# Performance work log

Measured on AMD Instinct MI355X. Metric: run time of the kernel, lower is better.

The kernel has to match this reference:

```python
import jax, jax.numpy as jnp
import numpy as np

N = 50000
E = 800000
IN_CH = 128
OUT_CH = 128
HEADS = 4
HEAD_DIM = OUT_CH // HEADS  # 32
NEG_SLOPE = 0.2
BN_EPS = 1e-5


def setup_inputs() -> dict:
    key = jax.random.key(0)
    ks = jax.random.split(key, 12)
    s = 1.0 / np.sqrt(IN_CH)
    x = jax.random.normal(ks[0], (N, IN_CH), dtype=jnp.float32)
    edge_index = jax.random.randint(ks[1], (2, E), 0, N, dtype=jnp.int64)
    # GATv2 lin_l (source) and lin_r (target) weights + biases
    W_l = jax.random.uniform(ks[2], (IN_CH, HEADS * HEAD_DIM), jnp.float32, -s, s)
    b_l = jax.random.uniform(ks[3], (HEADS * HEAD_DIM,), jnp.float32, -s, s)
    W_r = jax.random.uniform(ks[4], (IN_CH, HEADS * HEAD_DIM), jnp.float32, -s, s)
    b_r = jax.random.uniform(ks[5], (HEADS * HEAD_DIM,), jnp.float32, -s, s)
    att = jax.random.uniform(ks[6], (HEADS, HEAD_DIM), jnp.float32, -s, s)
    bias = jnp.zeros((HEADS * HEAD_DIM,), jnp.float32)
    gamma = jnp.ones((OUT_CH,), jnp.float32)
    beta = jnp.zeros((OUT_CH,), jnp.float32)
    return {"x": x, "edge_index": edge_index, "W_l": W_l, "b_l": b_l,
            "W_r": W_r, "b_r": b_r, "att": att, "bias": bias,
            "gamma": gamma, "beta": beta}


def gatv2_layer(x, edge_index, W_l, b_l, W_r, b_r, att, bias, gamma, beta):
    # transformed source/target features: [N, H, C]
    x_l = (x @ W_l + b_l).reshape(N, HEADS, HEAD_DIM)
    x_r = (x @ W_r + b_r).reshape(N, HEADS, HEAD_DIM)
    # add self loops
    loop = jnp.arange(N, dtype=edge_index.dtype)
    src = jnp.concatenate([edge_index[0], loop])
    dst = jnp.concatenate([edge_index[1], loop])
    # GATv2 attention scores per edge: a^T LeakyReLU(x_j + x_i)  -> [Etot, H]
    e = jax.nn.leaky_relu(x_l[src] + x_r[dst], NEG_SLOPE)
    score = jnp.einsum('ehc,hc->eh', e, att)
    # segment softmax over incoming edges of each destination node
    m = jax.ops.segment_max(score, dst, num_segments=N)
    ex = jnp.exp(score - m[dst])
    denom = jax.ops.segment_sum(ex, dst, num_segments=N)
    alpha = ex / denom[dst]
    # scatter-add aggregation of alpha * x_l[src]
    out = jax.ops.segment_sum(alpha[:, :, None] * x_l[src], dst, num_segments=N)
    out = out.reshape(N, OUT_CH) + bias
    # BatchNorm over nodes (training-mode batch statistics)
    mu = jnp.mean(out, axis=0)
    var = jnp.var(out, axis=0)
    out = (out - mu) / jnp.sqrt(var + BN_EPS) * gamma + beta
    # residual (in_channels == out_channels -> identity path) + ELU
    out = jax.nn.elu(out + x)
    return out


def reference(x, edge_index, W_l, b_l, W_r, b_r, att, bias, gamma, beta):
    return gatv2_layer(x, edge_index, W_l, b_l, W_r, b_r, att, bias, gamma, beta)
```

## Files before the change

kernel.cpp:

```cpp
#include <hip/hip_runtime.h>

#define NN 50000
#define EE 800000
#define ETOT (EE + NN)
#define GEMM_GRID 512
#define MTILES 782
#define COUNT_BLOCKS 3125
#define AGG_BLOCKS 1563
#define SCAN_BLOCKS 196

typedef __attribute__((ext_vector_type(8))) short bhalf8;
typedef __attribute__((ext_vector_type(4))) float fx4;

__device__ __forceinline__ unsigned bf16r(float f) {
  unsigned u = __float_as_uint(f);
  return (u + 0x7FFFu + ((u >> 16) & 1u)) >> 16;
}

__device__ __forceinline__ float4 unpack_bf16x4(unsigned a, unsigned b) {
  float4 f;
  f.x = __uint_as_float(a << 16);
  f.y = __uint_as_float(a & 0xFFFF0000u);
  f.z = __uint_as_float(b << 16);
  f.w = __uint_as_float(b & 0xFFFF0000u);
  return f;
}

__global__ __launch_bounds__(256) void gemm_count(
    const float* __restrict__ x,
    const float* __restrict__ Wl, const float* __restrict__ bl,
    const float* __restrict__ Wr, const float* __restrict__ br,
    unsigned short* __restrict__ xlh, float* __restrict__ xr,
    const int* __restrict__ ei, int* __restrict__ deg) {
  if (blockIdx.x >= GEMM_GRID) {
    int e = (blockIdx.x - GEMM_GRID) * 256 + threadIdx.x;
    if (e < EE) atomicAdd(&deg[ei[EE + e]], 1);
    return;
  }
  const int t = threadIdx.x;
  const int w = t >> 6;
  const int l = t & 63;
  const int cl = l & 15;
  const int kb = (l >> 4) * 8;
  const int rsub = (l >> 4) * 4;

  bhalf8 bfr[4][4];
  float biasv[4];
#pragma unroll
  for (int nt = 0; nt < 4; ++nt) {
    int col = w * 64 + nt * 16 + cl;
    const float* Wsrc;
    if (col < 128) { Wsrc = Wl + col; biasv[nt] = bl[col]; }
    else           { Wsrc = Wr + (col - 128); biasv[nt] = br[col - 128]; }
#pragma unroll
    for (int ch = 0; ch < 4; ++ch) {
      int k0 = ch * 32 + kb;
      bhalf8 f;
#pragma unroll
      for (int j = 0; j < 8; ++j)
        f[j] = (short)bf16r(Wsrc[(size_t)(k0 + j) * 128]);
      bfr[nt][ch] = f;
    }
  }

  for (int mt = blockIdx.x; mt < MTILES; mt += GEMM_GRID) {
    const int m0 = mt * 64;
#pragma unroll
    for (int rt = 0; rt < 4; ++rt) {
      int row = m0 + rt * 16 + cl;
      int rowc = row < NN ? row : NN - 1;
      const float* xp = x + (size_t)rowc * 128 + kb;
      bhalf8 afr[4];
#pragma unroll
      for (int ch = 0; ch < 4; ++ch) {
        float4 q0 = *(const float4*)(xp + ch * 32);
        float4 q1 = *(const float4*)(xp + ch * 32 + 4);
        bhalf8 f;
        f[0] = (short)bf16r(q0.x); f[1] = (short)bf16r(q0.y);
        f[2] = (short)bf16r(q0.z); f[3] = (short)bf16r(q0.w);
        f[4] = (short)bf16r(q1.x); f[5] = (short)bf16r(q1.y);
        f[6] = (short)bf16r(q1.z); f[7] = (short)bf16r(q1.w);
        afr[ch] = f;
      }
#pragma unroll
      for (int nt = 0; nt < 4; ++nt) {
        fx4 acc = {biasv[nt], biasv[nt], biasv[nt], biasv[nt]};
#pragma unroll
        for (int ch = 0; ch < 4; ++ch)
          acc = __builtin_amdgcn_mfma_f32_16x16x32_bf16(afr[ch], bfr[nt][ch],
                                                        acc, 0, 0, 0);
        int col = w * 64 + nt * 16 + cl;
        int rbase = m0 + rt * 16 + rsub;
        if (col < 128) {
#pragma unroll
          for (int r = 0; r < 4; ++r) {
            int rr = rbase + r;
            if (rr < NN) xlh[(size_t)rr * 128 + col] = (unsigned short)bf16r(acc[r]);
          }
        } else {
          int c2 = col - 128;
#pragma unroll
          for (int r = 0; r < 4; ++r) {
            int rr = rbase + r;
            if (rr < NN) xr[(size_t)rr * 128 + c2] = acc[r];
          }
        }
      }
    }
  }
}

__global__ __launch_bounds__(256) void scanA(const int* __restrict__ deg,
                                             int* __restrict__ bsum,
                                             float* __restrict__ bn) {
  __shared__ int s[256];
  int t = threadIdx.x;
  if (blockIdx.x == 0) bn[t] = 0.f;
  int i = blockIdx.x * 256 + t;
  s[t] = (i < NN) ? deg[i] : 0;
  __syncthreads();
#pragma unroll
  for (int off = 128; off > 0; off >>= 1) {
    if (t < off) s[t] += s[t + off];
    __syncthreads();
  }
  if (t == 0) bsum[blockIdx.x] = s[0];
}

__global__ __launch_bounds__(256) void scanB(const int* __restrict__ deg,
                                             const int* __restrict__ bsum,
                                             int* __restrict__ offs,
                                             int* __restrict__ cursor) {
  __shared__ int s[256];
  __shared__ int bpref;
  int t = threadIdx.x;
  int bid = blockIdx.x;
  int i = bid * 256 + t;
  int v = (i < NN) ? deg[i] : 0;
  s[t] = v;
  if (t == 0) {
    int r = 0;
    for (int k = 0; k < bid; ++k) r += bsum[k];
    bpref = r;
  }
  __syncthreads();
  for (int off = 1; off < 256; off <<= 1) {
    int u = (t >= off) ? s[t - off] : 0;
    __syncthreads();
    s[t] += u;
    __syncthreads();
  }
  int excl = s[t] - v + bpref;
  if (i <= NN) {
    offs[i] = excl;
    if (i < NN) cursor[i] = excl;
  }
}

__global__ void fill_csr(const int* __restrict__ ei, int* __restrict__ cursor,
                         int* __restrict__ csr) {
  int e = blockIdx.x * 256 + threadIdx.x;
  if (e >= ETOT) return;
  int s, d;
  if (e < EE) { s = ei[e]; d = ei[EE + e]; }
  else { s = e - EE; d = s; }
  int pos = atomicAdd(&cursor[d], 1);
  csr[pos] = s;
}

__global__ __launch_bounds__(256) void aggregate(
    const unsigned short* __restrict__ xlh, const float* __restrict__ xr,
    const int* __restrict__ offs, const int* __restrict__ csr,
    const float* __restrict__ att,
    float* __restrict__ out, float* __restrict__ bn) {
  __shared__ float sbn[256];
  int t = threadIdx.x;
  sbn[t] = 0.f;
  __syncthreads();
  const int lane = t & 63;
  const int gl = lane & 15;
  const int gb = lane & 48;
  const int c8 = gl * 8;
  const int gid = (blockIdx.x * 256 + t) >> 4;
  const int gstride = gridDim.x * 16;
  const float4 at0 = *(const float4*)&att[c8];
  const float4 at1 = *(const float4*)&att[c8 + 4];
  float4 bs0 = make_float4(0, 0, 0, 0), bs1 = make_float4(0, 0, 0, 0);
  float4 bq0 = make_float4(0, 0, 0, 0), bq1 = make_float4(0, 0, 0, 0);

  for (int node = gid; node < NN; node += gstride) {
    const float4 xr0 = *(const float4*)&xr[(size_t)node * 128 + c8];
    const float4 xr1 = *(const float4*)&xr[(size_t)node * 128 + c8 + 4];
    const int beg = offs[node];
    const int deg = offs[node + 1] - beg;
    float den = 0.f;
    float4 a0 = make_float4(0, 0, 0, 0), a1 = make_float4(0, 0, 0, 0);

    for (int base = 0; base < deg; base += 16) {
      int cnt = deg - base; if (cnt > 16) cnt = 16;
      int msrc = (gl < cnt) ? csr[beg + base + gl] : 0;
      for (int eb = 0; eb < cnt; eb += 8) {
        uint4 u[8];
#pragma unroll
        for (int j = 0; j < 8; ++j) {
          int s = __shfl(msrc, gb + eb + j, 64);
          u[j] = *(const uint4*)(xlh + (size_t)s * 128 + c8);
        }
#pragma unroll
        for (int j = 0; j < 8; ++j) {
          float4 v0 = unpack_bf16x4(u[j].x, u[j].y);
          float4 v1 = unpack_bf16x4(u[j].z, u[j].w);
          float e, p;
          e = v0.x + xr0.x; e = e > 0.f ? e : 0.2f * e; p = e * at0.x;
          e = v0.y + xr0.y; e = e > 0.f ? e : 0.2f * e; p = fmaf(e, at0.y, p);
          e = v0.z + xr0.z; e = e > 0.f ? e : 0.2f * e; p = fmaf(e, at0.z, p);
          e = v0.w + xr0.w; e = e > 0.f ? e : 0.2f * e; p = fmaf(e, at0.w, p);
          e = v1.x + xr1.x; e = e > 0.f ? e : 0.2f * e; p = fmaf(e, at1.x, p);
          e = v1.y + xr1.y; e = e > 0.f ? e : 0.2f * e; p = fmaf(e, at1.y, p);
          e = v1.z + xr1.z; e = e > 0.f ? e : 0.2f * e; p = fmaf(e, at1.z, p);
          e = v1.w + xr1.w; e = e > 0.f ? e : 0.2f * e; p = fmaf(e, at1.w, p);
          p += __shfl_xor(p, 1);
          p += __shfl_xor(p, 2);
          float pe = (eb + j < cnt) ? __expf(p) : 0.f;
          den += pe;
          a0.x = fmaf(pe, v0.x, a0.x);
          a0.y = fmaf(pe, v0.y, a0.y);
          a0.z = fmaf(pe, v0.z, a0.z);
          a0.w = fmaf(pe, v0.w, a0.w);
          a1.x = fmaf(pe, v1.x, a1.x);
          a1.y = fmaf(pe, v1.y, a1.y);
          a1.z = fmaf(pe, v1.z, a1.z);
          a1.w = fmaf(pe, v1.w, a1.w);
        }
      }
    }

    float inv = 1.0f / den;
    float4 r0, r1;
    r0.x = a0.x * inv; r0.y = a0.y * inv; r0.z = a0.z * inv; r0.w = a0.w * inv;
    r1.x = a1.x * inv; r1.y = a1.y * inv; r1.z = a1.z * inv; r1.w = a1.w * inv;
    *(float4*)&out[(size_t)node * 128 + c8] = r0;
    *(float4*)&out[(size_t)node * 128 + c8 + 4] = r1;
    bs0.x += r0.x; bs0.y += r0.y; bs0.z += r0.z; bs0.w += r0.w;
    bs1.x += r1.x; bs1.y += r1.y; bs1.z += r1.z; bs1.w += r1.w;
    bq0.x += r0.x * r0.x; bq0.y += r0.y * r0.y; bq0.z += r0.z * r0.z; bq0.w += r0.w * r0.w;
    bq1.x += r1.x * r1.x; bq1.y += r1.y * r1.y; bq1.z += r1.z * r1.z; bq1.w += r1.w * r1.w;
  }

#define RED(F) F = F + __shfl_xor(F, 16); F = F + __shfl_xor(F, 32);
  RED(bs0.x) RED(bs0.y) RED(bs0.z) RED(bs0.w)
  RED(bs1.x) RED(bs1.y) RED(bs1.z) RED(bs1.w)
  RED(bq0.x) RED(bq0.y) RED(bq0.z) RED(bq0.w)
  RED(bq1.x) RED(bq1.y) RED(bq1.z) RED(bq1.w)
#undef RED
  if (lane < 16) {
    atomicAdd(&sbn[c8 + 0], bs0.x);
    atomicAdd(&sbn[c8 + 1], bs0.y);
    atomicAdd(&sbn[c8 + 2], bs0.z);
    atomicAdd(&sbn[c8 + 3], bs0.w);
    atomicAdd(&sbn[c8 + 4], bs1.x);
    atomicAdd(&sbn[c8 + 5], bs1.y);
    atomicAdd(&sbn[c8 + 6], bs1.z);
    atomicAdd(&sbn[c8 + 7], bs1.w);
    atomicAdd(&sbn[128 + c8 + 0], bq0.x);
    atomicAdd(&sbn[128 + c8 + 1], bq0.y);
    atomicAdd(&sbn[128 + c8 + 2], bq0.z);
    atomicAdd(&sbn[128 + c8 + 3], bq0.w);
    atomicAdd(&sbn[128 + c8 + 4], bq1.x);
    atomicAdd(&sbn[128 + c8 + 5], bq1.y);
    atomicAdd(&sbn[128 + c8 + 6], bq1.z);
    atomicAdd(&sbn[128 + c8 + 7], bq1.w);
  }
  __syncthreads();
  atomicAdd(&bn[t], sbn[t]);
}

__global__ __launch_bounds__(256) void finalize(
    float* __restrict__ out, const float* __restrict__ x,
    const float* __restrict__ bn, const float* __restrict__ gamma,
    const float* __restrict__ beta) {
  __shared__ float smu[128], sgi[128];
  int t = threadIdx.x;
  if (t < 128) {
    float mu = bn[t] * (1.0f / NN);
    float var = bn[128 + t] * (1.0f / NN) - mu * mu;
    smu[t] = mu;
    sgi[t] = rsqrtf(var + 1e-5f) * gamma[t];
  }
  __syncthreads();
  const int total4 = NN * 32;
  for (int i = blockIdx.x * blockDim.x + threadIdx.x; i < total4;
       i += gridDim.x * blockDim.x) {
    int c4 = (i & 31) * 4;
    float4 o = ((const float4*)out)[i];
    float4 xv = ((const float4*)x)[i];
    float4 mu = *(const float4*)&smu[c4];
    float4 gi = *(const float4*)&sgi[c4];
    float4 b4 = *(const float4*)&beta[c4];
    float v;
    v = (o.x - mu.x) * gi.x + b4.x + xv.x; o.x = v > 0.f ? v : expm1f(v);
    v = (o.y - mu.y) * gi.y + b4.y + xv.y; o.y = v > 0.f ? v : expm1f(v);
    v = (o.z - mu.z) * gi.z + b4.z + xv.z; o.z = v > 0.f ? v : expm1f(v);
    v = (o.w - mu.w) * gi.w + b4.w + xv.w; o.w = v > 0.f ? v : expm1f(v);
    ((float4*)out)[i] = o;
  }
}

extern "C" void kernel_launch(void* const* d_in, const int* in_sizes, int n_in,
                              void* d_out, int out_size, void* d_ws, size_t ws_size,
                              hipStream_t stream) {
  const float* x    = (const float*)d_in[0];
  const int*   ei   = (const int*)d_in[1];
  const float* Wl   = (const float*)d_in[2];
  const float* bl   = (const float*)d_in[3];
  const float* Wr   = (const float*)d_in[4];
  const float* br   = (const float*)d_in[5];
  const float* att  = (const float*)d_in[6];
  const float* gam  = (const float*)d_in[8];
  const float* bet  = (const float*)d_in[9];
  float* out = (float*)d_out;

  unsigned short* xlh = (unsigned short*)d_ws;
  float* xr   = (float*)(xlh + (size_t)NN * 128);
  int* offs   = (int*)(xr + (size_t)NN * 128);
  int* cursor = offs + (NN + 4);
  int* deg    = cursor + NN;
  int* csr    = deg + NN;
  float* bn   = (float*)(csr + ETOT);
  int* bsum   = (int*)(bn + 256);

  hipMemsetD32Async((hipDeviceptr_t)deg, 1, NN, stream);

  hipLaunchKernelGGL(gemm_count, dim3(GEMM_GRID + COUNT_BLOCKS), dim3(256), 0,
                     stream, x, Wl, bl, Wr, br, xlh, xr, ei, deg);
  hipLaunchKernelGGL(scanA, dim3(SCAN_BLOCKS), dim3(256), 0, stream, deg, bsum, bn);
  hipLaunchKernelGGL(scanB, dim3(SCAN_BLOCKS), dim3(256), 0, stream,
                     deg, bsum, offs, cursor);
  hipLaunchKernelGGL(fill_csr, dim3((ETOT + 255) / 256), dim3(256), 0, stream,
                     ei, cursor, csr);
  hipLaunchKernelGGL(aggregate, dim3(AGG_BLOCKS), dim3(256), 0, stream,
                     xlh, xr, offs, csr, att, out, bn);
  hipLaunchKernelGGL(finalize, dim3(2048), dim3(256), 0, stream, out, x, bn, gam, bet);
}
```

Measured before the change: 298.8 us.

## Double-buffer edge gathers in aggregation and stage GEMM weights through LDS

The aggregation loop now processes up to 32 edges per chunk and double-buffers the bf16 source-feature gathers, issuing the next batch of 8 loads before consuming the current one. This hides gather latency behind the score and accumulate math. The GEMM block now loads W_l/W_r coalesced into a transposed bf16 LDS tile instead of doing strided scalar global reads per lane. Grid sizes for the GEMM and aggregation kernels are also retuned. The changes add register pressure from two 8-entry uint4 buffers and about 68KB of LDS per GEMM block, which may lower occupancy.

```diff
diff --git a/kernel.cpp b/kernel.cpp
--- a/kernel.cpp
+++ b/kernel.cpp
@@ -3,10 +3,10 @@
 #define NN 50000
 #define EE 800000
 #define ETOT (EE + NN)
-#define GEMM_GRID 512
+#define GEMM_GRID 391
 #define MTILES 782
 #define COUNT_BLOCKS 3125
-#define AGG_BLOCKS 1563
+#define AGG_BLOCKS 1024
 #define SCAN_BLOCKS 196
 
 typedef __attribute__((ext_vector_type(8))) short bhalf8;
@@ -37,6 +37,7 @@
     if (e < EE) atomicAdd(&deg[ei[EE + e]], 1);
     return;
   }
+  __shared__ unsigned short sW[256 * 136];
   const int t = threadIdx.x;
   const int w = t >> 6;
   const int l = t & 63;
@@ -44,23 +45,33 @@
   const int kb = (l >> 4) * 8;
   const int rsub = (l >> 4) * 4;
 
+#pragma unroll
+  for (int it = 0; it < 16; ++it) {
+    int f4 = t + it * 256;
+    int k = f4 >> 5;
+    int c4 = (f4 & 31) * 4;
+    float4 v = *(const float4*)&Wl[(size_t)k * 128 + c4];
+    sW[(c4 + 0) * 136 + k] = (unsigned short)bf16r(v.x);
+    sW[(c4 + 1) * 136 + k] = (unsigned short)bf16r(v.y);
+    sW[(c4 + 2) * 136 + k] = (unsigned short)bf16r(v.z);
+    sW[(c4 + 3) * 136 + k] = (unsigned short)bf16r(v.w);
+    float4 u = *(const float4*)&Wr[(size_t)k * 128 + c4];
+    sW[(128 + c4 + 0) * 136 + k] = (unsigned short)bf16r(u.x);
+    sW[(128 + c4 + 1) * 136 + k] = (unsigned short)bf16r(u.y);
+    sW[(128 + c4 + 2) * 136 + k] = (unsigned short)bf16r(u.z);
+    sW[(128 + c4 + 3) * 136 + k] = (unsigned short)bf16r(u.w);
+  }
+  __syncthreads();
+
   bhalf8 bfr[4][4];
   float biasv[4];
 #pragma unroll
   for (int nt = 0; nt < 4; ++nt) {
     int col = w * 64 + nt * 16 + cl;
-    const float* Wsrc;
-    if (col < 128) { Wsrc = Wl + col; biasv[nt] = bl[col]; }
-    else           { Wsrc = Wr + (col - 128); biasv[nt] = br[col - 128]; }
-#pragma unroll
-    for (int ch = 0; ch < 4; ++ch) {
-      int k0 = ch * 32 + kb;
-      bhalf8 f;
-#pragma unroll
-      for (int j = 0; j < 8; ++j)
-        f[j] = (short)bf16r(Wsrc[(size_t)(k0 + j) * 128]);
-      bfr[nt][ch] = f;
-    }
+    biasv[nt] = (col < 128) ? bl[col] : br[col - 128];
+#pragma unroll
+    for (int ch = 0; ch < 4; ++ch)
+      bfr[nt][ch] = *(const bhalf8*)&sW[col * 136 + ch * 32 + kb];
   }
 
   for (int mt = blockIdx.x; mt < MTILES; mt += GEMM_GRID) {
@@ -188,6 +199,45 @@
   float4 bs0 = make_float4(0, 0, 0, 0), bs1 = make_float4(0, 0, 0, 0);
   float4 bq0 = make_float4(0, 0, 0, 0), bq1 = make_float4(0, 0, 0, 0);
 
+#define LOADB(buf, bb) do {                                                   \
+    int mm = ((bb) >= 2) ? m1 : m0;                                           \
+    int ebase = gb + (((bb) & 1) << 3);                                       \
+    _Pragma("unroll")                                                         \
+    for (int j = 0; j < 8; ++j) {                                             \
+      int s = __shfl(mm, ebase + j, 64);                                      \
+      buf[j] = *(const uint4*)(xlh + (size_t)s * 128 + c8);                   \
+    }                                                                         \
+  } while (0)
+
+#define CONSUME(buf, bb) do {                                                 \
+    _Pragma("unroll")                                                         \
+    for (int j = 0; j < 8; ++j) {                                             \
+      float4 v0 = unpack_bf16x4(buf[j].x, buf[j].y);                          \
+      float4 v1 = unpack_bf16x4(buf[j].z, buf[j].w);                          \
+      float e, p;                                                             \
+      e = v0.x + xr0.x; e = e > 0.f ? e : 0.2f * e; p = e * at0.x;            \
+      e = v0.y + xr0.y; e = e > 0.f ? e : 0.2f * e; p = fmaf(e, at0.y, p);    \
+      e = v0.z + xr0.z; e = e > 0.f ? e : 0.2f * e; p = fmaf(e, at0.z, p);    \
+      e = v0.w + xr0.w; e = e > 0.f ? e : 0.2f * e; p = fmaf(e, at0.w, p);    \
+      e = v1.x + xr1.x; e = e > 0.f ? e : 0.2f * e; p = fmaf(e, at1.x, p);    \
+      e = v1.y + xr1.y; e = e > 0.f ? e : 0.2f * e; p = fmaf(e, at1.y, p);    \
+      e = v1.z + xr1.z; e = e > 0.f ? e : 0.2f * e; p = fmaf(e, at1.z, p);    \
+      e = v1.w + xr1.w; e = e > 0.f ? e : 0.2f * e; p = fmaf(e, at1.w, p);    \
+      p += __shfl_xor(p, 1);                                                  \
+      p += __shfl_xor(p, 2);                                                  \
+      float pe = ((bb) * 8 + j < rem) ? __expf(p) : 0.f;                      \
+      den += pe;                                                              \
+      a0.x = fmaf(pe, v0.x, a0.x);                                            \
+      a0.y = fmaf(pe, v0.y, a0.y);                                            \
+      a0.z = fmaf(pe, v0.z, a0.z);                                            \
+      a0.w = fmaf(pe, v0.w, a0.w);                                            \
+      a1.x = fmaf(pe, v1.x, a1.x);                                            \
+      a1.y = fmaf(pe, v1.y, a1.y);                                            \
+      a1.z = fmaf(pe, v1.z, a1.z);                                            \
+      a1.w = fmaf(pe, v1.w, a1.w);                                            \
+    }                                                                         \
+  } while (0)
+
   for (int node = gid; node < NN; node += gstride) {
     const float4 xr0 = *(const float4*)&xr[(size_t)node * 128 + c8];
     const float4 xr1 = *(const float4*)&xr[(size_t)node * 128 + c8 + 4];
@@ -196,42 +246,21 @@
     float den = 0.f;
     float4 a0 = make_float4(0, 0, 0, 0), a1 = make_float4(0, 0, 0, 0);
 
-    for (int base = 0; base < deg; base += 16) {
-      int cnt = deg - base; if (cnt > 16) cnt = 16;
-      int msrc = (gl < cnt) ? csr[beg + base + gl] : 0;
-      for (int eb = 0; eb < cnt; eb += 8) {
-        uint4 u[8];
-#pragma unroll
-        for (int j = 0; j < 8; ++j) {
-          int s = __shfl(msrc, gb + eb + j, 64);
-          u[j] = *(const uint4*)(xlh + (size_t)s * 128 + c8);
-        }
-#pragma unroll
-        for (int j = 0; j < 8; ++j) {
-          float4 v0 = unpack_bf16x4(u[j].x, u[j].y);
-          float4 v1 = unpack_bf16x4(u[j].z, u[j].w);
-          float e, p;
-          e = v0.x + xr0.x; e = e > 0.f ? e : 0.2f * e; p = e * at0.x;
-          e = v0.y + xr0.y; e = e > 0.f ? e : 0.2f * e; p = fmaf(e, at0.y, p);
-          e = v0.z + xr0.z; e = e > 0.f ? e : 0.2f * e; p = fmaf(e, at0.z, p);
-          e = v0.w + xr0.w; e = e > 0.f ? e : 0.2f * e; p = fmaf(e, at0.w, p);
-          e = v1.x + xr1.x; e = e > 0.f ? e : 0.2f * e; p = fmaf(e, at1.x, p);
-          e = v1.y + xr1.y; e = e > 0.f ? e : 0.2f * e; p = fmaf(e, at1.y, p);
-          e = v1.z + xr1.z; e = e > 0.f ? e : 0.2f * e; p = fmaf(e, at1.z, p);
-          e = v1.w + xr1.w; e = e > 0.f ? e : 0.2f * e; p = fmaf(e, at1.w, p);
-          p += __shfl_xor(p, 1);
-          p += __shfl_xor(p, 2);
-          float pe = (eb + j < cnt) ? __expf(p) : 0.f;
-          den += pe;
-          a0.x = fmaf(pe, v0.x, a0.x);
-          a0.y = fmaf(pe, v0.y, a0.y);
-          a0.z = fmaf(pe, v0.z, a0.z);
-          a0.w = fmaf(pe, v0.w, a0.w);
-          a1.x = fmaf(pe, v1.x, a1.x);
-          a1.y = fmaf(pe, v1.y, a1.y);
-          a1.z = fmaf(pe, v1.z, a1.z);
-          a1.w = fmaf(pe, v1.w, a1.w);
-        }
+    for (int base = 0; base < deg; base += 32) {
+      int rem = deg - base; if (rem > 32) rem = 32;
+      int m0 = (gl < rem)      ? csr[beg + base + gl]      : 0;
+      int m1 = (16 + gl < rem) ? csr[beg + base + 16 + gl] : 0;
+      int nb = (rem + 7) >> 3;
+      uint4 bufA[8], bufB[8];
+      LOADB(bufA, 0);
+      int b = 0;
+      for (;;) {
+        if (b + 1 < nb) LOADB(bufB, b + 1);
+        CONSUME(bufA, b);
+        if (++b >= nb) break;
+        if (b + 1 < nb) LOADB(bufA, b + 1);
+        CONSUME(bufB, b);
+        if (++b >= nb) break;
       }
     }
 
@@ -246,6 +275,8 @@
     bq0.x += r0.x * r0.x; bq0.y += r0.y * r0.y; bq0.z += r0.z * r0.z; bq0.w += r0.w * r0.w;
     bq1.x += r1.x * r1.x; bq1.y += r1.y * r1.y; bq1.z += r1.z * r1.z; bq1.w += r1.w * r1.w;
   }
+#undef LOADB
+#undef CONSUME
 
 #define RED(F) F = F + __shfl_xor(F, 16); F = F + __shfl_xor(F, 32);
   RED(bs0.x) RED(bs0.y) RED(bs0.z) RED(bs0.w)
```

Result: faster. 282.1 us (-5.6%).

## Pipeline neighbor gathers via async global-to-LDS loads and split out BN stats

Applied to the files above, without the earlier changes.

Restructures aggregate so each wave handles four nodes at once and streams neighbor feature rows into LDS with global_load_lds, keeping up to seven gathers in flight under explicit vmcnt waits. The BatchNorm sum and sum-of-squares reduction moves into a separate bn_stats kernel that rereads the output. The GEMM now stages transposed bf16 weights through shared memory instead of strided global loads, and the grid sizes change. The aim is to hide gather latency; the cost is an extra pass over the output, padded work when degrees in a group differ, and fragile hand-written waitcnt logic.

```diff
diff --git a/kernel.cpp b/kernel.cpp
--- a/kernel.cpp
+++ b/kernel.cpp
@@ -3,10 +3,10 @@
 #define NN 50000
 #define EE 800000
 #define ETOT (EE + NN)
-#define GEMM_GRID 512
+#define GEMM_GRID 391
 #define MTILES 782
 #define COUNT_BLOCKS 3125
-#define AGG_BLOCKS 1563
+#define AGG_BLOCKS 1280
 #define SCAN_BLOCKS 196
 
 typedef __attribute__((ext_vector_type(8))) short bhalf8;
@@ -25,6 +25,11 @@
   f.w = __uint_as_float(b & 0xFFFF0000u);
   return f;
 }
+
+#define GLOAD_LDS16(gp, lp)                                          \
+  __builtin_amdgcn_global_load_lds(                                  \
+      (const __attribute__((address_space(1))) void*)(gp),           \
+      (__attribute__((address_space(3))) void*)(lp), 16, 0, 0)
 
 __global__ __launch_bounds__(256) void gemm_count(
     const float* __restrict__ x,
@@ -37,6 +42,7 @@
     if (e < EE) atomicAdd(&deg[ei[EE + e]], 1);
     return;
   }
+  __shared__ unsigned short sW[256 * 136];
   const int t = threadIdx.x;
   const int w = t >> 6;
   const int l = t & 63;
@@ -44,23 +50,33 @@
   const int kb = (l >> 4) * 8;
   const int rsub = (l >> 4) * 4;
 
+#pragma unroll
+  for (int it = 0; it < 16; ++it) {
+    int f4 = t + it * 256;
+    int k = f4 >> 5;
+    int c4 = (f4 & 31) * 4;
+    float4 v = *(const float4*)&Wl[(size_t)k * 128 + c4];
+    sW[(c4 + 0) * 136 + k] = (unsigned short)bf16r(v.x);
+    sW[(c4 + 1) * 136 + k] = (unsigned short)bf16r(v.y);
+    sW[(c4 + 2) * 136 + k] = (unsigned short)bf16r(v.z);
+    sW[(c4 + 3) * 136 + k] = (unsigned short)bf16r(v.w);
+    float4 u = *(const float4*)&Wr[(size_t)k * 128 + c4];
+    sW[(128 + c4 + 0) * 136 + k] = (unsigned short)bf16r(u.x);
+    sW[(128 + c4 + 1) * 136 + k] = (unsigned short)bf16r(u.y);
+    sW[(128 + c4 + 2) * 136 + k] = (unsigned short)bf16r(u.z);
+    sW[(128 + c4 + 3) * 136 + k] = (unsigned short)bf16r(u.w);
+  }
+  __syncthreads();
+
   bhalf8 bfr[4][4];
   float biasv[4];
 #pragma unroll
   for (int nt = 0; nt < 4; ++nt) {
     int col = w * 64 + nt * 16 + cl;
-    const float* Wsrc;
-    if (col < 128) { Wsrc = Wl + col; biasv[nt] = bl[col]; }
-    else           { Wsrc = Wr + (col - 128); biasv[nt] = br[col - 128]; }
-#pragma unroll
-    for (int ch = 0; ch < 4; ++ch) {
-      int k0 = ch * 32 + kb;
-      bhalf8 f;
-#pragma unroll
-      for (int j = 0; j < 8; ++j)
-        f[j] = (short)bf16r(Wsrc[(size_t)(k0 + j) * 128]);
-      bfr[nt][ch] = f;
-    }
+    biasv[nt] = (col < 128) ? bl[col] : br[col - 128];
+#pragma unroll
+    for (int ch = 0; ch < 4; ++ch)
+      bfr[nt][ch] = *(const bhalf8*)&sW[col * 136 + ch * 32 + kb];
   }
 
   for (int mt = blockIdx.x; mt < MTILES; mt += GEMM_GRID) {
@@ -168,111 +184,156 @@
   csr[pos] = s;
 }
 
-__global__ __launch_bounds__(256) void aggregate(
+__global__ __launch_bounds__(256, 8) void aggregate(
     const unsigned short* __restrict__ xlh, const float* __restrict__ xr,
     const int* __restrict__ offs, const int* __restrict__ csr,
-    const float* __restrict__ att,
-    float* __restrict__ out, float* __restrict__ bn) {
-  __shared__ float sbn[256];
-  int t = threadIdx.x;
-  sbn[t] = 0.f;
-  __syncthreads();
-  const int lane = t & 63;
-  const int gl = lane & 15;
-  const int gb = lane & 48;
+    const float* __restrict__ att, float* __restrict__ out) {
+  __shared__ __align__(16) unsigned char stg[4][8][1024];
+  const int t = threadIdx.x;
+  const int w = t >> 6;
+  const int l = t & 63;
+  const int g = l >> 4;
+  const int gl = l & 15;
+  const int gb = l & 48;
   const int c8 = gl * 8;
-  const int gid = (blockIdx.x * 256 + t) >> 4;
-  const int gstride = gridDim.x * 16;
+  unsigned char* wbase = &stg[w][0][0];
   const float4 at0 = *(const float4*)&att[c8];
   const float4 at1 = *(const float4*)&att[c8 + 4];
-  float4 bs0 = make_float4(0, 0, 0, 0), bs1 = make_float4(0, 0, 0, 0);
-  float4 bq0 = make_float4(0, 0, 0, 0), bq1 = make_float4(0, 0, 0, 0);
-
-  for (int node = gid; node < NN; node += gstride) {
-    const float4 xr0 = *(const float4*)&xr[(size_t)node * 128 + c8];
-    const float4 xr1 = *(const float4*)&xr[(size_t)node * 128 + c8 + 4];
-    const int beg = offs[node];
-    const int deg = offs[node + 1] - beg;
+  const int wgid = blockIdx.x * 4 + w;
+  const int nstride = gridDim.x * 16;
+
+  for (int nb = wgid * 4; nb < NN; nb += nstride) {
+    const int node = nb + g;
+    const int nodec = node < NN ? node : NN - 1;
+    const float4 xr0 = *(const float4*)&xr[(size_t)nodec * 128 + c8];
+    const float4 xr1 = *(const float4*)&xr[(size_t)nodec * 128 + c8 + 4];
+    const int beg = offs[nodec];
+    int deg = offs[nodec + 1] - beg;
+    if (node >= NN) deg = 0;
+    int maxd = deg;
+    maxd = max(maxd, __shfl_xor(maxd, 16));
+    maxd = max(maxd, __shfl_xor(maxd, 32));
+
+    int m0, m1, m2, m3;
+    { int a = beg + gl;      a = a < ETOT ? a : ETOT - 1; m0 = csr[a]; }
+    m1 = m0; m2 = m0; m3 = m0;
+    if (maxd > 16) { int a = beg + 16 + gl; a = a < ETOT ? a : ETOT - 1; m1 = csr[a]; }
+    if (maxd > 32) { int a = beg + 32 + gl; a = a < ETOT ? a : ETOT - 1; m2 = csr[a]; }
+    if (maxd > 48) { int a = beg + 48 + gl; a = a < ETOT ? a : ETOT - 1; m3 = csr[a]; }
+
+    float xtouch = xr0.x + xr1.x;
+    asm volatile("" :: "v"(xtouch));
+
     float den = 0.f;
     float4 a0 = make_float4(0, 0, 0, 0), a1 = make_float4(0, 0, 0, 0);
 
-    for (int base = 0; base < deg; base += 16) {
-      int cnt = deg - base; if (cnt > 16) cnt = 16;
-      int msrc = (gl < cnt) ? csr[beg + base + gl] : 0;
-      for (int eb = 0; eb < cnt; eb += 8) {
-        uint4 u[8];
-#pragma unroll
-        for (int j = 0; j < 8; ++j) {
-          int s = __shfl(msrc, gb + eb + j, 64);
-          u[j] = *(const uint4*)(xlh + (size_t)s * 128 + c8);
-        }
-#pragma unroll
-        for (int j = 0; j < 8; ++j) {
-          float4 v0 = unpack_bf16x4(u[j].x, u[j].y);
-          float4 v1 = unpack_bf16x4(u[j].z, u[j].w);
-          float e, p;
-          e = v0.x + xr0.x; e = e > 0.f ? e : 0.2f * e; p = e * at0.x;
-          e = v0.y + xr0.y; e = e > 0.f ? e : 0.2f * e; p = fmaf(e, at0.y, p);
-          e = v0.z + xr0.z; e = e > 0.f ? e : 0.2f * e; p = fmaf(e, at0.z, p);
-          e = v0.w + xr0.w; e = e > 0.f ? e : 0.2f * e; p = fmaf(e, at0.w, p);
-          e = v1.x + xr1.x; e = e > 0.f ? e : 0.2f * e; p = fmaf(e, at1.x, p);
-          e = v1.y + xr1.y; e = e > 0.f ? e : 0.2f * e; p = fmaf(e, at1.y, p);
-          e = v1.z + xr1.z; e = e > 0.f ? e : 0.2f * e; p = fmaf(e, at1.z, p);
-          e = v1.w + xr1.w; e = e > 0.f ? e : 0.2f * e; p = fmaf(e, at1.w, p);
-          p += __shfl_xor(p, 1);
-          p += __shfl_xor(p, 2);
-          float pe = (eb + j < cnt) ? __expf(p) : 0.f;
-          den += pe;
-          a0.x = fmaf(pe, v0.x, a0.x);
-          a0.y = fmaf(pe, v0.y, a0.y);
-          a0.z = fmaf(pe, v0.z, a0.z);
-          a0.w = fmaf(pe, v0.w, a0.w);
-          a1.x = fmaf(pe, v1.x, a1.x);
-          a1.y = fmaf(pe, v1.y, a1.y);
-          a1.z = fmaf(pe, v1.z, a1.z);
-          a1.w = fmaf(pe, v1.w, a1.w);
-        }
-      }
+#define STAGE(i) do {                                                      \
+      int ii = (i);                                                        \
+      int cr = ii < 16 ? m0 : ii < 32 ? m1 : ii < 48 ? m2 : m3;            \
+      int s = __shfl(cr, gb + (ii & 15), 64);                              \
+      if (ii >= deg) s = 0;                                                \
+      GLOAD_LDS16(xlh + (size_t)s * 128 + c8,                              \
+                  wbase + (((unsigned)(ii)&7u) << 10));                    \
+    } while (0)
+
+#define CONSUME(i) do {                                                    \
+      uint4 u = *(const uint4*)(wbase + (((unsigned)(i)&7u) << 10) + l * 16); \
+      float4 v0 = unpack_bf16x4(u.x, u.y);                                 \
+      float4 v1 = unpack_bf16x4(u.z, u.w);                                 \
+      float e, p;                                                          \
+      e = v0.x + xr0.x; e = e > 0.f ? e : 0.2f * e; p = e * at0.x;         \
+      e = v0.y + xr0.y; e = e > 0.f ? e : 0.2f * e; p = fmaf(e, at0.y, p); \
+      e = v0.z + xr0.z; e = e > 0.f ? e : 0.2f * e; p = fmaf(e, at0.z, p); \
+      e = v0.w + xr0.w; e = e > 0.f ? e : 0.2f * e; p = fmaf(e, at0.w, p); \
+      e = v1.x + xr1.x; e = e > 0.f ? e : 0.2f * e; p = fmaf(e, at1.x, p); \
+      e = v1.y + xr1.y; e = e > 0.f ? e : 0.2f * e; p = fmaf(e, at1.y, p); \
+      e = v1.z + xr1.z; e = e > 0.f ? e : 0.2f * e; p = fmaf(e, at1.z, p); \
+      e = v1.w + xr1.w; e = e > 0.f ? e : 0.2f * e; p = fmaf(e, at1.w, p); \
+      p += __shfl_xor(p, 1);                                               \
+      p += __shfl_xor(p, 2);                                               \
+      float pe = ((i) < deg) ? __expf(p) : 0.f;                            \
+      den += pe;                                                           \
+      a0.x = fmaf(pe, v0.x, a0.x); a0.y = fmaf(pe, v0.y, a0.y);            \
+      a0.z = fmaf(pe, v0.z, a0.z); a0.w = fmaf(pe, v0.w, a0.w);            \
+      a1.x = fmaf(pe, v1.x, a1.x); a1.y = fmaf(pe, v1.y, a1.y);            \
+      a1.z = fmaf(pe, v1.z, a1.z); a1.w = fmaf(pe, v1.w, a1.w);            \
+    } while (0)
+
+    const int mp = maxd < 64 ? maxd : 64;
+    const int pro = mp < 7 ? mp : 7;
+    for (int i = 0; i < pro; ++i) STAGE(i);
+    const int me = mp - 7;
+    for (int i = 0; i < me; ++i) {
+      STAGE(i + 7);
+      asm volatile("s_waitcnt vmcnt(7)" ::: "memory");
+      CONSUME(i);
     }
-
-    float inv = 1.0f / den;
-    float4 r0, r1;
-    r0.x = a0.x * inv; r0.y = a0.y * inv; r0.z = a0.z * inv; r0.w = a0.w * inv;
-    r1.x = a1.x * inv; r1.y = a1.y * inv; r1.z = a1.z * inv; r1.w = a1.w * inv;
-    *(float4*)&out[(size_t)node * 128 + c8] = r0;
-    *(float4*)&out[(size_t)node * 128 + c8 + 4] = r1;
-    bs0.x += r0.x; bs0.y += r0.y; bs0.z += r0.z; bs0.w += r0.w;
-    bs1.x += r1.x; bs1.y += r1.y; bs1.z += r1.z; bs1.w += r1.w;
-    bq0.x += r0.x * r0.x; bq0.y += r0.y * r0.y; bq0.z += r0.z * r0.z; bq0.w += r0.w * r0.w;
-    bq1.x += r1.x * r1.x; bq1.y += r1.y * r1.y; bq1.z += r1.z * r1.z; bq1.w += r1.w * r1.w;
-  }
-
-#define RED(F) F = F + __shfl_xor(F, 16); F = F + __shfl_xor(F, 32);
-  RED(bs0.x) RED(bs0.y) RED(bs0.z) RED(bs0.w)
-  RED(bs1.x) RED(bs1.y) RED(bs1.z) RED(bs1.w)
-  RED(bq0.x) RED(bq0.y) RED(bq0.z) RED(bq0.w)
-  RED(bq1.x) RED(bq1.y) RED(bq1.z) RED(bq1.w)
-#undef RED
-  if (lane < 16) {
-    atomicAdd(&sbn[c8 + 0], bs0.x);
-    atomicAdd(&sbn[c8 + 1], bs0.y);
-    atomicAdd(&sbn[c8 + 2], bs0.z);
-    atomicAdd(&sbn[c8 + 3], bs0.w);
-    atomicAdd(&sbn[c8 + 4], bs1.x);
-    atomicAdd(&sbn[c8 + 5], bs1.y);
-    atomicAdd(&sbn[c8 + 6], bs1.z);
-    atomicAdd(&sbn[c8 + 7], bs1.w);
-    atomicAdd(&sbn[128 + c8 + 0], bq0.x);
-    atomicAdd(&sbn[128 + c8 + 1], bq0.y);
-    atomicAdd(&sbn[128 + c8 + 2], bq0.z);
-    atomicAdd(&sbn[128 + c8 + 3], bq0.w);
-    atomicAdd(&sbn[128 + c8 + 4], bq1.x);
-    atomicAdd(&sbn[128 + c8 + 5], bq1.y);
-    atomicAdd(&sbn[128 + c8 + 6], bq1.z);
-    atomicAdd(&sbn[128 + c8 + 7], bq1.w);
-  }
-  __syncthreads();
-  atomicAdd(&bn[t], sbn[t]);
+    asm volatile("s_waitcnt vmcnt(0)" ::: "memory");
+    for (int i = me > 0 ? me : 0; i < mp; ++i) CONSUME(i);
+
+    for (int i = 64; i < maxd; ++i) {
+      int a = beg + i; a = a < ETOT ? a : ETOT - 1;
+      int s = csr[a];
+      if (i >= deg) s = 0;
+      uint4 u = *(const uint4*)(xlh + (size_t)s * 128 + c8);
+      float4 v0 = unpack_bf16x4(u.x, u.y);
+      float4 v1 = unpack_bf16x4(u.z, u.w);
+      float e, p;
+      e = v0.x + xr0.x; e = e > 0.f ? e : 0.2f * e; p = e * at0.x;
+      e = v0.y + xr0.y; e = e > 0.f ? e : 0.2f * e; p = fmaf(e, at0.y, p);
+      e = v0.z + xr0.z; e = e > 0.f ? e : 0.2f * e; p = fmaf(e, at0.z, p);
+      e = v0.w + xr0.w; e = e > 0.f ? e : 0.2f * e; p = fmaf(e, at0.w, p);
+      e = v1.x + xr1.x; e = e > 0.f ? e : 0.2f * e; p = fmaf(e, at1.x, p);
+      e = v1.y + xr1.y; e = e > 0.f ? e : 0.2f * e; p = fmaf(e, at1.y, p);
+      e = v1.z + xr1.z; e = e > 0.f ? e : 0.2f * e; p = fmaf(e, at1.z, p);
+      e = v1.w + xr1.w; e = e > 0.f ? e : 0.2f * e; p = fmaf(e, at1.w, p);
+      p += __shfl_xor(p, 1);
+      p += __shfl_xor(p, 2);
+      float pe = (i < deg) ? __expf(p) : 0.f;
+      den += pe;
+      a0.x = fmaf(pe, v0.x, a0.x); a0.y = fmaf(pe, v0.y, a0.y);
+      a0.z = fmaf(pe, v0.z, a0.z); a0.w = fmaf(pe, v0.w, a0.w);
+      a1.x = fmaf(pe, v1.x, a1.x); a1.y = fmaf(pe, v1.y, a1.y);
+      a1.z = fmaf(pe, v1.z, a1.z); a1.w = fmaf(pe, v1.w, a1.w);
+    }
+#undef STAGE
+#undef CONSUME
+
+    if (node < NN) {
+      float inv = 1.0f / den;
+      float4 r0, r1;
+      r0.x = a0.x * inv; r0.y = a0.y * inv; r0.z = a0.z * inv; r0.w = a0.w * inv;
+      r1.x = a1.x * inv; r1.y = a1.y * inv; r1.z = a1.z * inv; r1.w = a1.w * inv;
+      *(float4*)&out[(size_t)node * 128 + c8] = r0;
+      *(float4*)&out[(size_t)node * 128 + c8 + 4] = r1;
+    }
+  }
+}
+
+__global__ __launch_bounds__(256) void bn_stats(const float* __restrict__ out,
+                                                float* __restrict__ bn) {
+  __shared__ float sb[256];
+  int t = threadIdx.x;
+  sb[t] = 0.f;
+  __syncthreads();
+  const int c4 = (t & 31) * 4;
+  float4 s = make_float4(0, 0, 0, 0), q = make_float4(0, 0, 0, 0);
+  const int total4 = NN * 32;
+  for (int i = blockIdx.x * 256 + t; i < total4; i += gridDim.x * 256) {
+    float4 o = ((const float4*)out)[i];
+    s.x += o.x; s.y += o.y; s.z += o.z; s.w += o.w;
+    q.x += o.x * o.x; q.y += o.y * o.y; q.z += o.z * o.z; q.w += o.w * o.w;
+  }
+  atomicAdd(&sb[c4 + 0], s.x);
+  atomicAdd(&sb[c4 + 1], s.y);
+  atomicAdd(&sb[c4 + 2], s.z);
+  atomicAdd(&sb[c4 + 3], s.w);
+  atomicAdd(&sb[128 + c4 + 0], q.x);
+  atomicAdd(&sb[128 + c4 + 1], q.y);
+  atomicAdd(&sb[128 + c4 + 2], q.z);
+  atomicAdd(&sb[128 + c4 + 3], q.w);
+  __syncthreads();
+  atomicAdd(&bn[t], sb[t]);
 }
 
 __global__ __launch_bounds__(256) void finalize(
@@ -339,6 +400,7 @@
   hipLaunchKernelGGL(fill_csr, dim3((ETOT + 255) / 256), dim3(256), 0, stream,
                      ei, cursor, csr);
   hipLaunchKernelGGL(aggregate, dim3(AGG_BLOCKS), dim3(256), 0, stream,
-                     xlh, xr, offs, csr, att, out, bn);
+                     xlh, xr, offs, csr, att, out);
+  hipLaunchKernelGGL(bn_stats, dim3(1024), dim3(256), 0, stream, out, bn);
   hipLaunchKernelGGL(finalize, dim3(2048), dim3(256), 0, stream, out, x, bn, gam, bet);
 }
```

New measurement: 313.0 us. 1.05x slower.
